# Performance work log

Hardware: AMD Instinct MI355X
Metric: run time of the kernel (lower is better)

## Reference

```python
import jax, jax.numpy as jnp
import numpy as np

T = 2048
HIDDEN = 4096
NQ = 32
NKV = 8
HD = 128
THETA = 10000.0


def setup_inputs() -> dict:
    key = jax.random.key(0)
    ks = jax.random.split(key, 5)
    s = 1.0 / np.sqrt(HIDDEN)
    return {
        "positions": jnp.arange(T, dtype=jnp.int32),
        "hidden_states": jax.random.normal(ks[0], (T, HIDDEN), dtype=jnp.float32),
        "wq": jax.random.normal(ks[1], (HIDDEN, NQ * HD), dtype=jnp.float32) * s,
        "wk": jax.random.normal(ks[2], (HIDDEN, NKV * HD), dtype=jnp.float32) * s,
        "wv": jax.random.normal(ks[3], (HIDDEN, NKV * HD), dtype=jnp.float32) * s,
        "wo": jax.random.normal(ks[4], (NQ * HD, HIDDEN), dtype=jnp.float32) * s,
    }


def _rope_neox(x, positions):
    # x: [T, H, HD]; neox style: split halves, rotate
    half = HD // 2
    inv_freq = 1.0 / (THETA ** (jnp.arange(0, half, dtype=jnp.float32) / half))
    ang = positions.astype(jnp.float32)[:, None] * inv_freq[None, :]  # [T, half]
    cos = jnp.cos(ang)[:, None, :]  # [T, 1, half]
    sin = jnp.sin(ang)[:, None, :]
    x1, x2 = x[..., :half], x[..., half:]
    return jnp.concatenate([x1 * cos - x2 * sin, x2 * cos + x1 * sin], axis=-1)


def reference(positions, hidden_states, wq, wk, wv, wo):
    scale = HD ** -0.5
    q = (hidden_states @ wq).reshape(T, NQ, HD)
    k = (hidden_states @ wk).reshape(T, NKV, HD)
    v = (hidden_states @ wv).reshape(T, NKV, HD)
    q = _rope_neox(q, positions)
    k = _rope_neox(k, positions)
    # GQA: repeat kv heads to match q heads
    group = NQ // NKV
    k_r = jnp.repeat(k, group, axis=1)  # [T, NQ, HD]
    v_r = jnp.repeat(v, group, axis=1)
    scores = jnp.einsum('qhd,khd->hqk', q, k_r) * scale  # [NQ, T, T]
    causal = positions[:, None] >= positions[None, :]  # [T, T]
    scores = jnp.where(causal[None, :, :], scores, -jnp.inf)
    probs = jax.nn.softmax(scores, axis=-1)
    attn = jnp.einsum('hqk,khd->qhd', probs, v_r).reshape(T, NQ * HD)
    return attn @ wo
```

## Files before the change

### kernel.cpp

```cpp
#include <hip/hip_runtime.h>

#define T_SEQ  2048
#define HID    4096
#define NQH    32
#define NKVH   8
#define HDIM   128

typedef float  f32x4  __attribute__((ext_vector_type(4)));
typedef __bf16 bf16x8 __attribute__((ext_vector_type(8)));

__device__ __forceinline__ float bf2f(unsigned short u) {
  union { unsigned int i; float f; } v; v.i = ((unsigned int)u) << 16; return v.f;
}
__device__ __forceinline__ unsigned short f2bf(float f) {
  union { float f; unsigned int i; } v; v.f = f;
  unsigned int r = v.i + 0x7fffu + ((v.i >> 16) & 1u);
  return (unsigned short)(r >> 16);
}

__device__ __forceinline__ f32x4 mfma_bf16(bf16x8 a, bf16x8 b, f32x4 c) {
  return __builtin_amdgcn_mfma_f32_16x16x32_bf16(a, b, c, 0, 0, 0);
}

#define GLOAD16(g, l)                                              \
  __builtin_amdgcn_global_load_lds(                                \
      (const __attribute__((address_space(1))) void*)(g),          \
      (__attribute__((address_space(3))) void*)(l), 16, 0, 0)

__global__ void prep_qw(const float* __restrict__ hs, unsigned short* __restrict__ hb,
                        const float* __restrict__ wq, unsigned short* __restrict__ wt) {
  __shared__ float tile[64][65];
  if (blockIdx.x < 8192) {
    long long i = ((long long)blockIdx.x * 256 + threadIdx.x) * 4;
    float4 v = *(const float4*)(hs + i);
    union { unsigned short u[4]; uint2 p; } o;
    o.u[0] = f2bf(v.x); o.u[1] = f2bf(v.y); o.u[2] = f2bf(v.z); o.u[3] = f2bf(v.w);
    *(uint2*)(hb + i) = o.p;
    return;
  }
  const int bid = blockIdx.x - 8192;
  const int N = NQH * HDIM, K = HID;
  int n0 = (bid & 63) * 64, k0 = (bid >> 6) * 64;
  int tx = threadIdx.x & 15, ty = threadIdx.x >> 4;
#pragma unroll
  for (int i = 0; i < 4; i++) {
    int k = ty + 16 * i;
    float4 f = *(const float4*)(wq + (long long)(k0 + k) * N + n0 + tx * 4);
    tile[tx * 4 + 0][k] = f.x;
    tile[tx * 4 + 1][k] = f.y;
    tile[tx * 4 + 2][k] = f.z;
    tile[tx * 4 + 3][k] = f.w;
  }
  __syncthreads();
#pragma unroll
  for (int i = 0; i < 4; i++) {
    int n = ty + 16 * i;
    union { unsigned short u[4]; uint2 p; } o;
    o.u[0] = f2bf(tile[n][tx * 4 + 0]);
    o.u[1] = f2bf(tile[n][tx * 4 + 1]);
    o.u[2] = f2bf(tile[n][tx * 4 + 2]);
    o.u[3] = f2bf(tile[n][tx * 4 + 3]);
    *(uint2*)(wt + (long long)(n0 + n) * K + k0 + tx * 4) = o.p;
  }
}

__global__ void transpose_conv(const float* __restrict__ W,
                               unsigned short* __restrict__ Wt, int K, int N) {
  __shared__ float tile[64][65];
  int n0 = blockIdx.x * 64, k0 = blockIdx.y * 64;
  int tx = threadIdx.x & 15, ty = threadIdx.x >> 4;
#pragma unroll
  for (int i = 0; i < 4; i++) {
    int k = ty + 16 * i;
    float4 f = *(const float4*)(W + (long long)(k0 + k) * N + n0 + tx * 4);
    tile[tx * 4 + 0][k] = f.x;
    tile[tx * 4 + 1][k] = f.y;
    tile[tx * 4 + 2][k] = f.z;
    tile[tx * 4 + 3][k] = f.w;
  }
  __syncthreads();
#pragma unroll
  for (int i = 0; i < 4; i++) {
    int n = ty + 16 * i;
    union { unsigned short u[4]; uint2 p; } o;
    o.u[0] = f2bf(tile[n][tx * 4 + 0]);
    o.u[1] = f2bf(tile[n][tx * 4 + 1]);
    o.u[2] = f2bf(tile[n][tx * 4 + 2]);
    o.u[3] = f2bf(tile[n][tx * 4 + 3]);
    *(uint2*)(Wt + (long long)(n0 + n) * K + k0 + tx * 4) = o.p;
  }
}

__global__ void transpose_conv_kv(const float* __restrict__ Wk,
                                  const float* __restrict__ Wv,
                                  unsigned short* __restrict__ Wt) {
  __shared__ float tile[64][65];
  const int N = NKVH * HDIM, K = HID;
  const float* W = blockIdx.z ? Wv : Wk;
  unsigned short* dst = Wt + (size_t)blockIdx.z * N * K;
  int n0 = blockIdx.x * 64, k0 = blockIdx.y * 64;
  int tx = threadIdx.x & 15, ty = threadIdx.x >> 4;
#pragma unroll
  for (int i = 0; i < 4; i++) {
    int k = ty + 16 * i;
    float4 f = *(const float4*)(W + (long long)(k0 + k) * N + n0 + tx * 4);
    tile[tx * 4 + 0][k] = f.x;
    tile[tx * 4 + 1][k] = f.y;
    tile[tx * 4 + 2][k] = f.z;
    tile[tx * 4 + 3][k] = f.w;
  }
  __syncthreads();
#pragma unroll
  for (int i = 0; i < 4; i++) {
    int n = ty + 16 * i;
    union { unsigned short u[4]; uint2 p; } o;
    o.u[0] = f2bf(tile[n][tx * 4 + 0]);
    o.u[1] = f2bf(tile[n][tx * 4 + 1]);
    o.u[2] = f2bf(tile[n][tx * 4 + 2]);
    o.u[3] = f2bf(tile[n][tx * 4 + 3]);
    *(uint2*)(dst + (long long)(n0 + n) * K + k0 + tx * 4) = o.p;
  }
}

template <int EPI>
__global__ __launch_bounds__(256) void gemm_bt(const unsigned short* __restrict__ A,
                                               const unsigned short* __restrict__ Bt,
                                               void* __restrict__ Cv,
                                               int M, int N, int K) {
  __shared__ unsigned short As[128 * 64];
  __shared__ unsigned short Bs[128 * 64];
  const int lin = blockIdx.y * gridDim.x + blockIdx.x;
  const int cpx = (gridDim.x * gridDim.y) >> 3;
  const int swz = (lin & 7) * cpx + (lin >> 3);
  const int bx = swz % gridDim.x, by = swz / gridDim.x;

  const int t = threadIdx.x;
  const int lane = t & 63, w = t >> 6;
  const int wr = w >> 1, wc = w & 1;
  const int l15 = lane & 15, lg = lane >> 4;
  const int m0 = by * 128, n0 = bx * 128;

  f32x4 acc[4][4];
#pragma unroll
  for (int i = 0; i < 4; i++)
#pragma unroll
    for (int j = 0; j < 4; j++) acc[i][j] = (f32x4){0.f, 0.f, 0.f, 0.f};

  for (int kt = 0; kt < K; kt += 64) {
    __syncthreads();
#pragma unroll
    for (int s = 0; s < 4; s++) {
      int c = t + s * 256;
      int row = c >> 3, sub = c & 7;
      GLOAD16(A + (long long)(m0 + row) * K + kt + ((sub ^ (row & 7)) * 8),
              (char*)As + (w * 64 + s * 256) * 16);
      GLOAD16(Bt + (long long)(n0 + row) * K + kt + ((sub ^ (row & 7)) * 8),
              (char*)Bs + (w * 64 + s * 256) * 16);
    }
    __syncthreads();

#pragma unroll
    for (int kk = 0; kk < 2; kk++) {
      bf16x8 af[4], bfr[4];
#pragma unroll
      for (int mi = 0; mi < 4; mi++) {
        int row = wr * 64 + mi * 16 + l15;
        af[mi] = *(const bf16x8*)(As + row * 64 + (((kk * 4 + lg) ^ (row & 7)) * 8));
      }
#pragma unroll
      for (int ni = 0; ni < 4; ni++) {
        int row = wc * 64 + ni * 16 + l15;
        bfr[ni] = *(const bf16x8*)(Bs + row * 64 + (((kk * 4 + lg) ^ (row & 7)) * 8));
      }
#pragma unroll
      for (int mi = 0; mi < 4; mi++)
#pragma unroll
        for (int ni = 0; ni < 4; ni++)
          acc[mi][ni] = mfma_bf16(af[mi], bfr[ni], acc[mi][ni]);
    }
  }

  const int row0 = m0 + wr * 64, col0 = n0 + wc * 64;
#pragma unroll
  for (int mi = 0; mi < 4; mi++)
#pragma unroll
    for (int ni = 0; ni < 4; ni++) {
      int rbase = row0 + mi * 16 + lg * 4;
      int col = col0 + ni * 16 + l15;
#pragma unroll
      for (int r = 0; r < 4; r++) {
        float v = acc[mi][ni][r];
        if (EPI == 0)
          ((unsigned short*)Cv)[(long long)(rbase + r) * N + col] = f2bf(v);
        else
          ((float*)Cv)[(long long)(rbase + r) * N + col] = v;
      }
    }
}

__global__ __launch_bounds__(256) void gemm_kv64(const unsigned short* __restrict__ A,
                                                 const unsigned short* __restrict__ Bt,
                                                 unsigned short* __restrict__ Ckv,
                                                 unsigned short* __restrict__ Cvt) {
  __shared__ unsigned short As[64 * 64];
  __shared__ unsigned short Bs[128 * 64];
  __shared__ unsigned short Tt[128 * 64];
  const int lin = blockIdx.y * gridDim.x + blockIdx.x;
  const int swz = (lin & 7) * 64 + (lin >> 3);
  const int bx = swz & 15, by = swz >> 4;

  const int t = threadIdx.x;
  const int lane = t & 63, w = t >> 6;
  const int wr = w >> 1, wc = w & 1;
  const int l15 = lane & 15, lg = lane >> 4;
  const int m0 = by * 64, n0 = bx * 128;
  const int K = HID;

  f32x4 acc[2][4];
#pragma unroll
  for (int i = 0; i < 2; i++)
#pragma unroll
    for (int j = 0; j < 4; j++) acc[i][j] = (f32x4){0.f, 0.f, 0.f, 0.f};

  for (int kt = 0; kt < K; kt += 64) {
    __syncthreads();
#pragma unroll
    for (int s = 0; s < 2; s++) {
      int c = t + s * 256;
      int row = c >> 3, sub = c & 7;
      GLOAD16(A + (long long)(m0 + row) * K + kt + ((sub ^ (row & 7)) * 8),
              (char*)As + (w * 64 + s * 256) * 16);
    }
#pragma unroll
    for (int s = 0; s < 4; s++) {
      int c = t + s * 256;
      int row = c >> 3, sub = c & 7;
      GLOAD16(Bt + (long long)(n0 + row) * K + kt + ((sub ^ (row & 7)) * 8),
              (char*)Bs + (w * 64 + s * 256) * 16);
    }
    __syncthreads();

#pragma unroll
    for (int kk = 0; kk < 2; kk++) {
      bf16x8 af[2], bfr[4];
#pragma unroll
      for (int mi = 0; mi < 2; mi++) {
        int row = wr * 32 + mi * 16 + l15;
        af[mi] = *(const bf16x8*)(As + row * 64 + (((kk * 4 + lg) ^ (row & 7)) * 8));
      }
#pragma unroll
      for (int ni = 0; ni < 4; ni++) {
        int row = wc * 64 + ni * 16 + l15;
        bfr[ni] = *(const bf16x8*)(Bs + row * 64 + (((kk * 4 + lg) ^ (row & 7)) * 8));
      }
#pragma unroll
      for (int mi = 0; mi < 2; mi++)
#pragma unroll
        for (int ni = 0; ni < 4; ni++)
          acc[mi][ni] = mfma_bf16(af[mi], bfr[ni], acc[mi][ni]);
    }
  }

  const int row0 = m0 + wr * 32, col0 = n0 + wc * 64;
  if (n0 < 1024) {
#pragma unroll
    for (int mi = 0; mi < 2; mi++)
#pragma unroll
      for (int ni = 0; ni < 4; ni++) {
        int rbase = row0 + mi * 16 + lg * 4;
        int col = col0 + ni * 16 + l15;
#pragma unroll
        for (int r = 0; r < 4; r++)
          Ckv[(long long)(rbase + r) * 1024 + col] = f2bf(acc[mi][ni][r]);
      }
  } else {
#pragma unroll
    for (int mi = 0; mi < 2; mi++)
#pragma unroll
      for (int ni = 0; ni < 4; ni++) {
        int nloc = wc * 64 + ni * 16 + l15;
#pragma unroll
        for (int r = 0; r < 4; r++) {
          int mloc = wr * 32 + mi * 16 + lg * 4 + r;
          Tt[nloc * 64 + (mloc ^ ((nloc & 7) << 3))] = f2bf(acc[mi][ni][r]);
        }
      }
    __syncthreads();
    const int nloc = t >> 1;
#pragma unroll
    for (int cc = 0; cc < 4; cc++) {
      int ci = (t & 1) * 4 + cc;
      int sc = ci ^ (nloc & 7);
      uint4 v = *(const uint4*)(Tt + nloc * 64 + sc * 8);
      *(uint4*)(Cvt + (long long)(n0 - 1024 + nloc) * T_SEQ + m0 + ci * 8) = v;
    }
  }
}

__global__ void rope_all(unsigned short* __restrict__ qb,
                         unsigned short* __restrict__ kb,
                         const int* __restrict__ positions) {
  const int w = threadIdx.x >> 6, d = threadIdx.x & 63;
  const int gid = blockIdx.x * 4 + w;
  unsigned short* row;
  int t;
  bool isq;
  if (gid < T_SEQ * NQH) {
    int h = gid & (NQH - 1); t = gid >> 5;
    row = qb + (size_t)t * (NQH * HDIM) + (size_t)h * HDIM;
    isq = true;
  } else {
    int g = gid - T_SEQ * NQH;
    int h = g & (NKVH - 1); t = g >> 3;
    row = kb + (size_t)t * (NKVH * HDIM) + (size_t)h * HDIM;
    isq = false;
  }
  double inv = exp2(-(double)d * 0.20762050593046014);
  double ang = (double)positions[t] * inv;
  double c = cos(ang), s = sin(ang);
  if (isq) { c *= 0.12751744416986895; s *= 0.12751744416986895; }
  float x1 = bf2f(row[d]), x2 = bf2f(row[d + 64]);
  row[d]      = f2bf((float)((double)x1 * c - (double)x2 * s));
  row[d + 64] = f2bf((float)((double)x2 * c + (double)x1 * s));
}

__global__ __launch_bounds__(256) void attn_kernel(const unsigned short* __restrict__ qb,
                                                   const unsigned short* __restrict__ kb,
                                                   const unsigned short* __restrict__ vt,
                                                   unsigned short* __restrict__ ab) {
  __shared__ unsigned short Ks[64 * 128];
  __shared__ unsigned short Vs[128 * 64];
  __shared__ unsigned short Ps[4][16 * 64];

  const int lin = blockIdx.y * gridDim.x + blockIdx.x;
  const int swz = (lin & 7) * 128 + (lin >> 3);
  const int bx = swz & 63;
  const int hp = swz >> 6;
  const int kvh = hp >> 1;
  const int t = threadIdx.x, lane = t & 63, w = t >> 6;
  const int l15 = lane & 15, lg = lane >> 4;
  const int head = 2 * hp + (w & 1);
  const int wr16 = (w >> 1) * 16;
  const int jt = (hp & 1) ? bx : 63 - bx;
  const int q0 = jt * 32;

  bf16x8 qf[4];
#pragma unroll
  for (int kk = 0; kk < 4; kk++)
    qf[kk] = *(const bf16x8*)(qb + (long long)(q0 + wr16 + l15) * (NQH * HDIM) +
                              head * HDIM + kk * 32 + lg * 8);

  f32x4 accO[8];
#pragma unroll
  for (int db = 0; db < 8; db++) accO[db] = (f32x4){0.f, 0.f, 0.f, 0.f};
  float mrun[4] = {-3e38f, -3e38f, -3e38f, -3e38f};
  float lrun[4] = {0.f, 0.f, 0.f, 0.f};

  const int jd = jt >> 1;
  const int nt = jd + 1;
  for (int kt = 0; kt < nt; kt++) {
    __syncthreads();
#pragma unroll
    for (int s = 0; s < 4; s++) {
      int c = t + s * 256;
      int row = c >> 4, chk = c & 15;
      GLOAD16(kb + (long long)(kt * 64 + row) * (NKVH * HDIM) + kvh * HDIM +
                  ((chk ^ (row & 7)) * 8),
              (char*)Ks + (w * 64 + s * 256) * 16);
    }
#pragma unroll
    for (int s = 0; s < 4; s++) {
      int c = t + s * 256;
      int row = c >> 3, chk = c & 7;
      GLOAD16(vt + (long long)(kvh * HDIM + row) * T_SEQ + kt * 64 +
                  ((chk ^ (row & 7)) * 8),
              (char*)Vs + (w * 64 + s * 256) * 16);
    }
    __syncthreads();

    f32x4 accS[4];
#pragma unroll
    for (int kc = 0; kc < 4; kc++) accS[kc] = (f32x4){0.f, 0.f, 0.f, 0.f};
    __builtin_amdgcn_s_setprio(1);
#pragma unroll
    for (int kk = 0; kk < 4; kk++)
#pragma unroll
      for (int kc = 0; kc < 4; kc++) {
        int row = kc * 16 + l15;
        bf16x8 b = *(const bf16x8*)(Ks + row * 128 + (((kk * 4 + lg) ^ (l15 & 7)) * 8));
        accS[kc] = mfma_bf16(qf[kk], b, accS[kc]);
      }
    __builtin_amdgcn_s_setprio(0);

    float pm[4][4];
    if (kt == jd) {
      const int qloc = (jt & 1) * 32 + wr16 + lg * 4;
#pragma unroll
      for (int kc = 0; kc < 4; kc++) {
        int kcl = kc * 16 + l15;
#pragma unroll
        for (int r = 0; r < 4; r++)
          pm[kc][r] = (kcl > qloc + r) ? -3e38f : accS[kc][r];
      }
    } else {
#pragma unroll
      for (int kc = 0; kc < 4; kc++)
#pragma unroll
        for (int r = 0; r < 4; r++) pm[kc][r] = accS[kc][r];
    }

    float rm[4];
#pragma unroll
    for (int r = 0; r < 4; r++)
      rm[r] = fmaxf(fmaxf(pm[0][r], pm[1][r]), fmaxf(pm[2][r], pm[3][r]));
    int needl = 0;
#pragma unroll
    for (int r = 0; r < 4; r++) needl |= (rm[r] > mrun[r] + 8.f) ? 1 : 0;
    if (__any(needl)) {
#pragma unroll
      for (int off = 1; off < 16; off <<= 1)
#pragma unroll
        for (int r = 0; r < 4; r++) rm[r] = fmaxf(rm[r], __shfl_xor(rm[r], off, 64));
#pragma unroll
      for (int r = 0; r < 4; r++) {
        float mn = fmaxf(mrun[r], rm[r]);
        float corr = exp2f(mrun[r] - mn);
        mrun[r] = mn;
        lrun[r] *= corr;
#pragma unroll
        for (int db = 0; db < 8; db++) accO[db][r] *= corr;
      }
    }

    __bf16 pbh[4][4];
#pragma unroll
    for (int kc = 0; kc < 4; kc++)
#pragma unroll
      for (int r = 0; r < 4; r++) {
        float p = exp2f(pm[kc][r] - mrun[r]);
        lrun[r] += p;
        pbh[kc][r] = (__bf16)p;
      }

    unsigned short* Pw = &Ps[w][0];
#pragma unroll
    for (int kc = 0; kc < 4; kc++)
#pragma unroll
      for (int r = 0; r < 4; r++) {
        int prow = lg * 4 + r;
        ((__bf16*)Pw)[(prow * 64 + kc * 16 + l15) ^ ((prow & 7) << 3)] = pbh[kc][r];
      }
    asm volatile("s_waitcnt lgkmcnt(0)" ::: "memory");

    __builtin_amdgcn_s_setprio(1);
#pragma unroll
    for (int ks = 0; ks < 2; ks++) {
      bf16x8 pa = *(const bf16x8*)(Pw + ((l15 * 64 + ks * 32 + lg * 8) ^ ((l15 & 7) << 3)));
#pragma unroll
      for (int db = 0; db < 8; db++) {
        int vrow = db * 16 + l15;
        bf16x8 b = *(const bf16x8*)(Vs + vrow * 64 + (((ks * 4 + lg) ^ (vrow & 7)) * 8));
        accO[db] = mfma_bf16(pa, b, accO[db]);
      }
    }
    __builtin_amdgcn_s_setprio(0);
  }

#pragma unroll
  for (int off = 1; off < 16; off <<= 1)
#pragma unroll
    for (int r = 0; r < 4; r++) lrun[r] += __shfl_xor(lrun[r], off, 64);
#pragma unroll
  for (int db = 0; db < 8; db++)
#pragma unroll
    for (int r = 0; r < 4; r++) {
      int qr = q0 + wr16 + lg * 4 + r;
      int col = head * HDIM + db * 16 + l15;
      ((__bf16*)ab)[(long long)qr * (NQH * HDIM) + col] = (__bf16)(accO[db][r] / lrun[r]);
    }
}

extern "C" void kernel_launch(void* const* d_in, const int* in_sizes, int n_in,
                              void* d_out, int out_size, void* d_ws, size_t ws_size,
                              hipStream_t stream) {
  const int*   positions = (const int*)d_in[0];
  const float* hs = (const float*)d_in[1];
  const float* wq = (const float*)d_in[2];
  const float* wk = (const float*)d_in[3];
  const float* wv = (const float*)d_in[4];
  const float* wo = (const float*)d_in[5];
  float* out = (float*)d_out;

  const size_t SZ_WT = (size_t)HID * HID * 2;
  const size_t SZ_HB = (size_t)T_SEQ * HID * 2;
  const size_t SZ_QB = (size_t)T_SEQ * NQH * HDIM * 2;
  const size_t SZ_KB = (size_t)T_SEQ * NKVH * HDIM * 2;
  const size_t need = SZ_WT + SZ_HB + SZ_QB + SZ_KB * 2;
  if (ws_size < need) return;

  char* p = (char*)d_ws;
  unsigned short* wt  = (unsigned short*)p; p += SZ_WT;
  unsigned short* hb  = (unsigned short*)p; p += SZ_HB;
  unsigned short* qb  = (unsigned short*)p; p += SZ_QB;
  unsigned short* kb  = (unsigned short*)p; p += SZ_KB;
  unsigned short* vtb = (unsigned short*)p; p += SZ_KB;
  unsigned short* ab  = hb;

  prep_qw<<<8192 + 4096, 256, 0, stream>>>(hs, hb, wq, wt);
  gemm_bt<0><<<dim3((NQH * HDIM) / 128, T_SEQ / 128), 256, 0, stream>>>(hb, wt, qb, T_SEQ, NQH * HDIM, HID);

  transpose_conv_kv<<<dim3((NKVH * HDIM) / 64, HID / 64, 2), 256, 0, stream>>>(wk, wv, wt);
  gemm_kv64<<<dim3(16, 32), 256, 0, stream>>>(hb, wt, kb, vtb);

  rope_all<<<(T_SEQ * (NQH + NKVH)) / 4, 256, 0, stream>>>(qb, kb, positions);

  attn_kernel<<<dim3(64, 16), 256, 0, stream>>>(qb, kb, vtb, ab);

  transpose_conv<<<dim3(HID / 64, (NQH * HDIM) / 64), 256, 0, stream>>>(wo, wt, NQH * HDIM, HID);
  gemm_bt<2><<<dim3(HID / 128, T_SEQ / 128), 256, 0, stream>>>(ab, wt, out, T_SEQ, HID, NQH * HDIM);
}
```

Measured before the change: 391.1 us.

## Pair complementary causal query tiles per block to balance attention work

Measured after the change: 400.2 us. 1.02x slower.

```diff
diff --git a/kernel.cpp b/kernel.cpp
--- a/kernel.cpp
+++ b/kernel.cpp
@@ -324,41 +324,136 @@
   row[d + 64] = f2bf((float)((double)x2 * c + (double)x1 * s));
 }
 
+__device__ __forceinline__ void attn_body(const unsigned short* __restrict__ Ksb,
+                                          const unsigned short* __restrict__ Vsb,
+                                          unsigned short* __restrict__ Pw,
+                                          const bf16x8 qf[4], f32x4 accO[8],
+                                          float mrun[4], float lrun[4],
+                                          bool diag, int w16, int l15, int lg) {
+  f32x4 accS[4];
+#pragma unroll
+  for (int kc = 0; kc < 4; kc++) accS[kc] = (f32x4){0.f, 0.f, 0.f, 0.f};
+  __builtin_amdgcn_s_setprio(1);
+#pragma unroll
+  for (int kk = 0; kk < 4; kk++)
+#pragma unroll
+    for (int kc = 0; kc < 4; kc++) {
+      int row = kc * 16 + l15;
+      bf16x8 b = *(const bf16x8*)(Ksb + row * 128 + (((kk * 4 + lg) ^ (l15 & 7)) * 8));
+      accS[kc] = mfma_bf16(qf[kk], b, accS[kc]);
+    }
+  __builtin_amdgcn_s_setprio(0);
+
+  float pm[4][4];
+  if (diag) {
+    const int qloc = w16 + lg * 4;
+#pragma unroll
+    for (int kc = 0; kc < 4; kc++) {
+      int kcl = kc * 16 + l15;
+#pragma unroll
+      for (int r = 0; r < 4; r++)
+        pm[kc][r] = (kcl > qloc + r) ? -3e38f : accS[kc][r];
+    }
+  } else {
+#pragma unroll
+    for (int kc = 0; kc < 4; kc++)
+#pragma unroll
+      for (int r = 0; r < 4; r++) pm[kc][r] = accS[kc][r];
+  }
+
+  float rm[4];
+#pragma unroll
+  for (int r = 0; r < 4; r++)
+    rm[r] = fmaxf(fmaxf(pm[0][r], pm[1][r]), fmaxf(pm[2][r], pm[3][r]));
+  int needl = 0;
+#pragma unroll
+  for (int r = 0; r < 4; r++) needl |= (rm[r] > mrun[r] + 8.f) ? 1 : 0;
+  if (__any(needl)) {
+#pragma unroll
+    for (int off = 1; off < 16; off <<= 1)
+#pragma unroll
+      for (int r = 0; r < 4; r++) rm[r] = fmaxf(rm[r], __shfl_xor(rm[r], off, 64));
+#pragma unroll
+    for (int r = 0; r < 4; r++) {
+      float mn = fmaxf(mrun[r], rm[r]);
+      float corr = exp2f(mrun[r] - mn);
+      mrun[r] = mn;
+      lrun[r] *= corr;
+#pragma unroll
+      for (int db = 0; db < 8; db++) accO[db][r] *= corr;
+    }
+  }
+
+  __bf16 pbh[4][4];
+#pragma unroll
+  for (int kc = 0; kc < 4; kc++)
+#pragma unroll
+    for (int r = 0; r < 4; r++) {
+      float p = exp2f(pm[kc][r] - mrun[r]);
+      lrun[r] += p;
+      pbh[kc][r] = (__bf16)p;
+    }
+
+#pragma unroll
+  for (int kc = 0; kc < 4; kc++)
+#pragma unroll
+    for (int r = 0; r < 4; r++) {
+      int prow = lg * 4 + r;
+      ((__bf16*)Pw)[(prow * 64 + kc * 16 + l15) ^ ((prow & 7) << 3)] = pbh[kc][r];
+    }
+  asm volatile("s_waitcnt lgkmcnt(0)" ::: "memory");
+
+  __builtin_amdgcn_s_setprio(1);
+#pragma unroll
+  for (int ks = 0; ks < 2; ks++) {
+    bf16x8 pa = *(const bf16x8*)(Pw + ((l15 * 64 + ks * 32 + lg * 8) ^ ((l15 & 7) << 3)));
+#pragma unroll
+    for (int db = 0; db < 8; db++) {
+      int vrow = db * 16 + l15;
+      bf16x8 b = *(const bf16x8*)(Vsb + vrow * 64 + (((ks * 4 + lg) ^ (vrow & 7)) * 8));
+      accO[db] = mfma_bf16(pa, b, accO[db]);
+    }
+  }
+  __builtin_amdgcn_s_setprio(0);
+}
+
 __global__ __launch_bounds__(256) void attn_kernel(const unsigned short* __restrict__ qb,
                                                    const unsigned short* __restrict__ kb,
                                                    const unsigned short* __restrict__ vt,
                                                    unsigned short* __restrict__ ab) {
   __shared__ unsigned short Ks[64 * 128];
   __shared__ unsigned short Vs[128 * 64];
-  __shared__ unsigned short Ps[4][16 * 64];
+  __shared__ unsigned short Ps[4][2][16 * 64];
 
   const int lin = blockIdx.y * gridDim.x + blockIdx.x;
-  const int swz = (lin & 7) * 128 + (lin >> 3);
-  const int bx = swz & 63;
-  const int hp = swz >> 6;
-  const int kvh = hp >> 1;
+  const int swz = (lin & 7) * 64 + (lin >> 3);
+  const int bx = swz & 15;
+  const int h  = swz >> 4;
+  const int kvh = h >> 2;
+  const int jA = 31 - bx, jB = bx;
+  const int q0A = jA * 64, q0B = jB * 64;
   const int t = threadIdx.x, lane = t & 63, w = t >> 6;
   const int l15 = lane & 15, lg = lane >> 4;
-  const int head = 2 * hp + (w & 1);
-  const int wr16 = (w >> 1) * 16;
-  const int jt = (hp & 1) ? bx : 63 - bx;
-  const int q0 = jt * 32;
-
-  bf16x8 qf[4];
-#pragma unroll
-  for (int kk = 0; kk < 4; kk++)
-    qf[kk] = *(const bf16x8*)(qb + (long long)(q0 + wr16 + l15) * (NQH * HDIM) +
-                              head * HDIM + kk * 32 + lg * 8);
-
-  f32x4 accO[8];
-#pragma unroll
-  for (int db = 0; db < 8; db++) accO[db] = (f32x4){0.f, 0.f, 0.f, 0.f};
-  float mrun[4] = {-3e38f, -3e38f, -3e38f, -3e38f};
-  float lrun[4] = {0.f, 0.f, 0.f, 0.f};
-
-  const int jd = jt >> 1;
-  const int nt = jd + 1;
-  for (int kt = 0; kt < nt; kt++) {
+
+  bf16x8 qfA[4], qfB[4];
+#pragma unroll
+  for (int kk = 0; kk < 4; kk++) {
+    qfA[kk] = *(const bf16x8*)(qb + (long long)(q0A + w * 16 + l15) * (NQH * HDIM) +
+                               h * HDIM + kk * 32 + lg * 8);
+    qfB[kk] = *(const bf16x8*)(qb + (long long)(q0B + w * 16 + l15) * (NQH * HDIM) +
+                               h * HDIM + kk * 32 + lg * 8);
+  }
+
+  f32x4 accA[8], accB[8];
+#pragma unroll
+  for (int db = 0; db < 8; db++) {
+    accA[db] = (f32x4){0.f, 0.f, 0.f, 0.f};
+    accB[db] = (f32x4){0.f, 0.f, 0.f, 0.f};
+  }
+  float mA[4] = {-3e38f, -3e38f, -3e38f, -3e38f}, lA[4] = {0.f, 0.f, 0.f, 0.f};
+  float mB[4] = {-3e38f, -3e38f, -3e38f, -3e38f}, lB[4] = {0.f, 0.f, 0.f, 0.f};
+
+  for (int kt = 0; kt <= jA; kt++) {
     __syncthreads();
 #pragma unroll
     for (int s = 0; s < 4; s++) {
@@ -378,105 +473,29 @@
     }
     __syncthreads();
 
-    f32x4 accS[4];
-#pragma unroll
-    for (int kc = 0; kc < 4; kc++) accS[kc] = (f32x4){0.f, 0.f, 0.f, 0.f};
-    __builtin_amdgcn_s_setprio(1);
-#pragma unroll
-    for (int kk = 0; kk < 4; kk++)
-#pragma unroll
-      for (int kc = 0; kc < 4; kc++) {
-        int row = kc * 16 + l15;
-        bf16x8 b = *(const bf16x8*)(Ks + row * 128 + (((kk * 4 + lg) ^ (l15 & 7)) * 8));
-        accS[kc] = mfma_bf16(qf[kk], b, accS[kc]);
-      }
-    __builtin_amdgcn_s_setprio(0);
-
-    float pm[4][4];
-    if (kt == jd) {
-      const int qloc = (jt & 1) * 32 + wr16 + lg * 4;
-#pragma unroll
-      for (int kc = 0; kc < 4; kc++) {
-        int kcl = kc * 16 + l15;
-#pragma unroll
-        for (int r = 0; r < 4; r++)
-          pm[kc][r] = (kcl > qloc + r) ? -3e38f : accS[kc][r];
-      }
-    } else {
-#pragma unroll
-      for (int kc = 0; kc < 4; kc++)
-#pragma unroll
-        for (int r = 0; r < 4; r++) pm[kc][r] = accS[kc][r];
-    }
-
-    float rm[4];
-#pragma unroll
-    for (int r = 0; r < 4; r++)
-      rm[r] = fmaxf(fmaxf(pm[0][r], pm[1][r]), fmaxf(pm[2][r], pm[3][r]));
-    int needl = 0;
-#pragma unroll
-    for (int r = 0; r < 4; r++) needl |= (rm[r] > mrun[r] + 8.f) ? 1 : 0;
-    if (__any(needl)) {
-#pragma unroll
-      for (int off = 1; off < 16; off <<= 1)
-#pragma unroll
-        for (int r = 0; r < 4; r++) rm[r] = fmaxf(rm[r], __shfl_xor(rm[r], off, 64));
-#pragma unroll
-      for (int r = 0; r < 4; r++) {
-        float mn = fmaxf(mrun[r], rm[r]);
-        float corr = exp2f(mrun[r] - mn);
-        mrun[r] = mn;
-        lrun[r] *= corr;
-#pragma unroll
-        for (int db = 0; db < 8; db++) accO[db][r] *= corr;
-      }
-    }
-
-    __bf16 pbh[4][4];
-#pragma unroll
-    for (int kc = 0; kc < 4; kc++)
-#pragma unroll
-      for (int r = 0; r < 4; r++) {
-        float p = exp2f(pm[kc][r] - mrun[r]);
-        lrun[r] += p;
-        pbh[kc][r] = (__bf16)p;
-      }
-
-    unsigned short* Pw = &Ps[w][0];
-#pragma unroll
-    for (int kc = 0; kc < 4; kc++)
-#pragma unroll
-      for (int r = 0; r < 4; r++) {
-        int prow = lg * 4 + r;
-        ((__bf16*)Pw)[(prow * 64 + kc * 16 + l15) ^ ((prow & 7) << 3)] = pbh[kc][r];
-      }
-    asm volatile("s_waitcnt lgkmcnt(0)" ::: "memory");
-
-    __builtin_amdgcn_s_setprio(1);
-#pragma unroll
-    for (int ks = 0; ks < 2; ks++) {
-      bf16x8 pa = *(const bf16x8*)(Pw + ((l15 * 64 + ks * 32 + lg * 8) ^ ((l15 & 7) << 3)));
-#pragma unroll
-      for (int db = 0; db < 8; db++) {
-        int vrow = db * 16 + l15;
-        bf16x8 b = *(const bf16x8*)(Vs + vrow * 64 + (((ks * 4 + lg) ^ (vrow & 7)) * 8));
-        accO[db] = mfma_bf16(pa, b, accO[db]);
-      }
-    }
-    __builtin_amdgcn_s_setprio(0);
+    attn_body(Ks, Vs, (unsigned short*)&Ps[w][0][0], qfA, accA, mA, lA,
+              kt == jA, w * 16, l15, lg);
+    if (kt <= jB)
+      attn_body(Ks, Vs, (unsigned short*)&Ps[w][1][0], qfB, accB, mB, lB,
+                kt == jB, w * 16, l15, lg);
   }
 
 #pragma unroll
   for (int off = 1; off < 16; off <<= 1)
 #pragma unroll
-    for (int r = 0; r < 4; r++) lrun[r] += __shfl_xor(lrun[r], off, 64);
+    for (int r = 0; r < 4; r++) {
+      lA[r] += __shfl_xor(lA[r], off, 64);
+      lB[r] += __shfl_xor(lB[r], off, 64);
+    }
 #pragma unroll
   for (int db = 0; db < 8; db++)
 #pragma unroll
     for (int r = 0; r < 4; r++) {
-      int qr = q0 + wr16 + lg * 4 + r;
-      int col = head * HDIM + db * 16 + l15;
-      ((__bf16*)ab)[(long long)qr * (NQH * HDIM) + col] = (__bf16)(accO[db][r] / lrun[r]);
+      int col = h * HDIM + db * 16 + l15;
+      int qrA = q0A + w * 16 + lg * 4 + r;
+      int qrB = q0B + w * 16 + lg * 4 + r;
+      ((__bf16*)ab)[(long long)qrA * (NQH * HDIM) + col] = (__bf16)(accA[db][r] / lA[r]);
+      ((__bf16*)ab)[(long long)qrB * (NQH * HDIM) + col] = (__bf16)(accB[db][r] / lB[r]);
     }
 }
 
@@ -514,7 +533,7 @@
 
   rope_all<<<(T_SEQ * (NQH + NKVH)) / 4, 256, 0, stream>>>(qb, kb, positions);
 
-  attn_kernel<<<dim3(64, 16), 256, 0, stream>>>(qb, kb, vtb, ab);
+  attn_kernel<<<dim3(16, 32), 256, 0, stream>>>(qb, kb, vtb, ab);
 
   transpose_conv<<<dim3(HID / 64, (NQH * HDIM) / 64), 256, 0, stream>>>(wo, wt, NQH * HDIM, HID);
   gemm_bt<2><<<dim3(HID / 128, T_SEQ / 128), 256, 0, stream>>>(ab, wt, out, T_SEQ, HID, NQH * HDIM);
```

## Compute transposed S tile to keep P in registers, removing LDS round-trip

Applied to the files above, without the earlier changes.

Measured after the change: 390.5 us. No clear change (-0.2%).

```diff
diff --git a/kernel.cpp b/kernel.cpp
--- a/kernel.cpp
+++ b/kernel.cpp
@@ -8,6 +8,7 @@
 
 typedef float  f32x4  __attribute__((ext_vector_type(4)));
 typedef __bf16 bf16x8 __attribute__((ext_vector_type(8)));
+typedef __bf16 bf16x4 __attribute__((ext_vector_type(4)));
 
 __device__ __forceinline__ float bf2f(unsigned short u) {
   union { unsigned int i; float f; } v; v.i = ((unsigned int)u) << 16; return v.f;
@@ -330,7 +331,6 @@
                                                    unsigned short* __restrict__ ab) {
   __shared__ unsigned short Ks[64 * 128];
   __shared__ unsigned short Vs[128 * 64];
-  __shared__ unsigned short Ps[4][16 * 64];
 
   const int lin = blockIdx.y * gridDim.x + blockIdx.x;
   const int swz = (lin & 7) * 128 + (lin >> 3);
@@ -353,12 +353,10 @@
   f32x4 accO[8];
 #pragma unroll
   for (int db = 0; db < 8; db++) accO[db] = (f32x4){0.f, 0.f, 0.f, 0.f};
-  float mrun[4] = {-3e38f, -3e38f, -3e38f, -3e38f};
-  float lrun[4] = {0.f, 0.f, 0.f, 0.f};
+  float mrun = -3e38f, lrun = 0.f;
 
   const int jd = jt >> 1;
-  const int nt = jd + 1;
-  for (int kt = 0; kt < nt; kt++) {
+  for (int kt = 0; kt <= jd; kt++) {
     __syncthreads();
 #pragma unroll
     for (int s = 0; s < 4; s++) {
@@ -387,21 +385,19 @@
 #pragma unroll
       for (int kc = 0; kc < 4; kc++) {
         int row = kc * 16 + l15;
-        bf16x8 b = *(const bf16x8*)(Ks + row * 128 + (((kk * 4 + lg) ^ (l15 & 7)) * 8));
-        accS[kc] = mfma_bf16(qf[kk], b, accS[kc]);
+        bf16x8 a = *(const bf16x8*)(Ks + row * 128 + (((kk * 4 + lg) ^ (l15 & 7)) * 8));
+        accS[kc] = mfma_bf16(a, qf[kk], accS[kc]);
       }
     __builtin_amdgcn_s_setprio(0);
 
     float pm[4][4];
     if (kt == jd) {
-      const int qloc = (jt & 1) * 32 + wr16 + lg * 4;
-#pragma unroll
-      for (int kc = 0; kc < 4; kc++) {
-        int kcl = kc * 16 + l15;
+      const int qloc = (jt & 1) * 32 + wr16 + l15;
+#pragma unroll
+      for (int kc = 0; kc < 4; kc++)
 #pragma unroll
         for (int r = 0; r < 4; r++)
-          pm[kc][r] = (kcl > qloc + r) ? -3e38f : accS[kc][r];
-      }
+          pm[kc][r] = (kc * 16 + lg * 4 + r > qloc) ? -3e38f : accS[kc][r];
     } else {
 #pragma unroll
       for (int kc = 0; kc < 4; kc++)
@@ -409,74 +405,77 @@
         for (int r = 0; r < 4; r++) pm[kc][r] = accS[kc][r];
     }
 
-    float rm[4];
-#pragma unroll
-    for (int r = 0; r < 4; r++)
-      rm[r] = fmaxf(fmaxf(pm[0][r], pm[1][r]), fmaxf(pm[2][r], pm[3][r]));
-    int needl = 0;
-#pragma unroll
-    for (int r = 0; r < 4; r++) needl |= (rm[r] > mrun[r] + 8.f) ? 1 : 0;
-    if (__any(needl)) {
-#pragma unroll
-      for (int off = 1; off < 16; off <<= 1)
-#pragma unroll
-        for (int r = 0; r < 4; r++) rm[r] = fmaxf(rm[r], __shfl_xor(rm[r], off, 64));
+    float rm = pm[0][0];
+#pragma unroll
+    for (int kc = 0; kc < 4; kc++)
+#pragma unroll
+      for (int r = 0; r < 4; r++) rm = fmaxf(rm, pm[kc][r]);
+    if (__any(rm > mrun + 8.f)) {
+      rm = fmaxf(rm, __shfl_xor(rm, 16, 64));
+      rm = fmaxf(rm, __shfl_xor(rm, 32, 64));
+      float mn = fmaxf(mrun, rm);
+      float corr = exp2f(mrun - mn);
+      mrun = mn;
+      lrun *= corr;
+      float cO[4];
+#pragma unroll
+      for (int r = 0; r < 4; r++) cO[r] = __shfl(corr, lg * 4 + r, 64);
+#pragma unroll
+      for (int db = 0; db < 8; db++)
+#pragma unroll
+        for (int r = 0; r < 4; r++) accO[db][r] *= cO[r];
+    }
+
+    float p[4][4];
+#pragma unroll
+    for (int kc = 0; kc < 4; kc++)
 #pragma unroll
       for (int r = 0; r < 4; r++) {
-        float mn = fmaxf(mrun[r], rm[r]);
-        float corr = exp2f(mrun[r] - mn);
-        mrun[r] = mn;
-        lrun[r] *= corr;
-#pragma unroll
-        for (int db = 0; db < 8; db++) accO[db][r] *= corr;
-      }
-    }
-
-    __bf16 pbh[4][4];
-#pragma unroll
-    for (int kc = 0; kc < 4; kc++)
-#pragma unroll
-      for (int r = 0; r < 4; r++) {
-        float p = exp2f(pm[kc][r] - mrun[r]);
-        lrun[r] += p;
-        pbh[kc][r] = (__bf16)p;
-      }
-
-    unsigned short* Pw = &Ps[w][0];
-#pragma unroll
-    for (int kc = 0; kc < 4; kc++)
-#pragma unroll
-      for (int r = 0; r < 4; r++) {
-        int prow = lg * 4 + r;
-        ((__bf16*)Pw)[(prow * 64 + kc * 16 + l15) ^ ((prow & 7) << 3)] = pbh[kc][r];
-      }
-    asm volatile("s_waitcnt lgkmcnt(0)" ::: "memory");
-
+        p[kc][r] = exp2f(pm[kc][r] - mrun);
+        lrun += p[kc][r];
+      }
+    bf16x8 pa0, pa1;
+#pragma unroll
+    for (int j = 0; j < 8; j++) {
+      pa0[j] = (__bf16)p[(j >> 2)][j & 3];
+      pa1[j] = (__bf16)p[2 + (j >> 2)][j & 3];
+    }
+
+    const int swl = l15 & 7;
+    const int coff = (lg & 1) * 4;
+    const int c80 = lg >> 1;
     __builtin_amdgcn_s_setprio(1);
 #pragma unroll
-    for (int ks = 0; ks < 2; ks++) {
-      bf16x8 pa = *(const bf16x8*)(Pw + ((l15 * 64 + ks * 32 + lg * 8) ^ ((l15 & 7) << 3)));
-#pragma unroll
-      for (int db = 0; db < 8; db++) {
-        int vrow = db * 16 + l15;
-        bf16x8 b = *(const bf16x8*)(Vs + vrow * 64 + (((ks * 4 + lg) ^ (vrow & 7)) * 8));
-        accO[db] = mfma_bf16(pa, b, accO[db]);
-      }
+    for (int db = 0; db < 8; db++) {
+      int vb = (db * 16 + l15) * 64;
+      union { bf16x8 v; bf16x4 h[2]; } b;
+      b.h[0] = *(const bf16x4*)(Vs + vb + ((c80 ^ swl) * 8 + coff));
+      b.h[1] = *(const bf16x4*)(Vs + vb + (((c80 + 2) ^ swl) * 8 + coff));
+      accO[db] = mfma_bf16(pa0, b.v, accO[db]);
+    }
+#pragma unroll
+    for (int db = 0; db < 8; db++) {
+      int vb = (db * 16 + l15) * 64;
+      union { bf16x8 v; bf16x4 h[2]; } b;
+      b.h[0] = *(const bf16x4*)(Vs + vb + (((c80 + 4) ^ swl) * 8 + coff));
+      b.h[1] = *(const bf16x4*)(Vs + vb + (((c80 + 6) ^ swl) * 8 + coff));
+      accO[db] = mfma_bf16(pa1, b.v, accO[db]);
     }
     __builtin_amdgcn_s_setprio(0);
   }
 
-#pragma unroll
-  for (int off = 1; off < 16; off <<= 1)
-#pragma unroll
-    for (int r = 0; r < 4; r++) lrun[r] += __shfl_xor(lrun[r], off, 64);
+  lrun += __shfl_xor(lrun, 16, 64);
+  lrun += __shfl_xor(lrun, 32, 64);
+  float lO[4];
+#pragma unroll
+  for (int r = 0; r < 4; r++) lO[r] = __shfl(lrun, lg * 4 + r, 64);
 #pragma unroll
   for (int db = 0; db < 8; db++)
 #pragma unroll
     for (int r = 0; r < 4; r++) {
       int qr = q0 + wr16 + lg * 4 + r;
       int col = head * HDIM + db * 16 + l15;
-      ((__bf16*)ab)[(long long)qr * (NQH * HDIM) + col] = (__bf16)(accO[db][r] / lrun[r]);
+      ((__bf16*)ab)[(long long)qr * (NQH * HDIM) + col] = (__bf16)(accO[db][r] / lO[r]);
     }
 }
 
```
